# Kernel optimization log

Measured on AMD Instinct MI355X. Metric: run time of the kernel, lower is better.

## Reference

```python
import jax, jax.numpy as jnp
import numpy as np

WS = 7          # window_size
NUM_HEADS = 8
EPS = 1e-5


def _layernorm(x, g, b):
    m = jnp.mean(x, axis=-1, keepdims=True)
    v = jnp.var(x, axis=-1, keepdims=True)
    return (x - m) * jax.lax.rsqrt(v + EPS) * g + b


def _window_attention(win, w_qkv, b_qkv, w_proj, b_proj):
    B_, L, C = win.shape
    h = NUM_HEADS
    d = C // h
    scale = d ** -0.5
    qkv = win @ w_qkv.T + b_qkv                      # (B_, L, 3C)
    qkv = qkv.reshape(B_, L, 3, h, d).transpose(2, 0, 3, 1, 4)  # (3, B_, h, L, d)
    q, k, v = qkv[0], qkv[1], qkv[2]
    attn = jnp.einsum('bhld,bhmd->bhlm', q, k) * scale
    attn = jax.nn.softmax(attn, axis=-1)
    out = jnp.einsum('bhlm,bhmd->bhld', attn, v)     # (B_, h, L, d)
    out = out.transpose(0, 2, 1, 3).reshape(B_, L, C)
    return out @ w_proj.T + b_proj


def _forward(x, H, W, g1, b1, w_qkv, b_qkv, w_proj, b_proj, g2, b2,
             w_fc1, b_fc1, w_fc2, b_fc2):
    N, L, C = x.shape
    shortcut = x
    y = _layernorm(x, g1, b1).reshape(N, H, W, C)
    pad_h = (WS - H % WS) % WS
    pad_w = (WS - W % WS) % WS
    y = jnp.pad(y, ((0, 0), (0, pad_h), (0, pad_w), (0, 0)))
    Hp, Wp = H + pad_h, W + pad_w
    # window partition: (N, Hp/WS, WS, Wp/WS, WS, C) -> (N*nW, WS*WS, C)
    y = y.reshape(N, Hp // WS, WS, Wp // WS, WS, C).transpose(0, 1, 3, 2, 4, 5)
    windows = y.reshape(-1, WS * WS, C)
    attn_windows = _window_attention(windows, w_qkv, b_qkv, w_proj, b_proj)
    # window reverse
    y = attn_windows.reshape(N, Hp // WS, Wp // WS, WS, WS, C)
    y = y.transpose(0, 1, 3, 2, 4, 5).reshape(N, Hp, Wp, C)[:, :H, :W, :]
    y = y.reshape(N, H * W, C)
    x = shortcut + y
    # MLP: Linear -> GELU (erf, torch default) -> Linear
    z = _layernorm(x, g2, b2)
    z = jax.nn.gelu(z @ w_fc1.T + b_fc1, approximate=False) @ w_fc2.T + b_fc2
    return x + z


def setup_inputs() -> dict:
    key = jax.random.key(0)
    ks = jax.random.split(key, 8)
    N, H, W, C = 8, 112, 112, 256
    hidden = 4 * C
    s = 0.02
    return {
        'x': jax.random.normal(ks[0], (N, H * W, C), jnp.float32),
        'H': H,
        'W': W,
        'g1': jnp.ones((C,), jnp.float32),
        'b1': jnp.zeros((C,), jnp.float32),
        'w_qkv': jax.random.normal(ks[1], (3 * C, C), jnp.float32) * s,
        'b_qkv': jnp.zeros((3 * C,), jnp.float32),
        'w_proj': jax.random.normal(ks[2], (C, C), jnp.float32) * s,
        'b_proj': jnp.zeros((C,), jnp.float32),
        'g2': jnp.ones((C,), jnp.float32),
        'b2': jnp.zeros((C,), jnp.float32),
        'w_fc1': jax.random.normal(ks[3], (hidden, C), jnp.float32) * s,
        'b_fc1': jnp.zeros((hidden,), jnp.float32),
        'w_fc2': jax.random.normal(ks[4], (C, hidden), jnp.float32) * s,
        'b_fc2': jnp.zeros((C,), jnp.float32),
    }


def reference(x, H, W, g1, b1, w_qkv, b_qkv, w_proj, b_proj, g2, b2,
              w_fc1, b_fc1, w_fc2, b_fc2):
    return _forward(x, H, W, g1, b1, w_qkv, b_qkv, w_proj, b_proj,
                    g2, b2, w_fc1, b_fc1, w_fc2, b_fc2)
```

## Files before the change

### kernel.cpp

```cpp
#include <hip/hip_runtime.h>
#include <hip/hip_bf16.h>
#include <cstdint>
#include <cstddef>


typedef __bf16 bf16x8 __attribute__((ext_vector_type(8)));
typedef float f32x4 __attribute__((ext_vector_type(4)));

__device__ __forceinline__ unsigned short f2bf(float f){
    union{float f;uint32_t u;}c;c.f=f;uint32_t u=c.u;u+=0x7fffu+((u>>16)&1u);return (unsigned short)(u>>16);}
__device__ __forceinline__ float gelu_f(float x){ return 0.5f*x*(1.0f+erff(x*0.70710678118654752f)); }
__device__ __forceinline__ int swz(int row,int g){ return (g & ~7) | ((g ^ row) & 7); }

__global__ __launch_bounds__(256) void conv_k(
    const float* __restrict__ src, unsigned short* __restrict__ dst, int n4)
{
    int i = blockIdx.x * 256 + threadIdx.x;
    if (i >= n4) return;
    float4 v = *(const float4*)(src + (size_t)i * 4);
    uint2 o;
    o.x = (uint32_t)f2bf(v.x) | ((uint32_t)f2bf(v.y) << 16);
    o.y = (uint32_t)f2bf(v.z) | ((uint32_t)f2bf(v.w) << 16);
    *(uint2*)(dst + (size_t)i * 4) = o;
}

__global__ __launch_bounds__(512, 2) void attn_half_k(
    const float* __restrict__ x, const float* __restrict__ g1, const float* __restrict__ b1,
    const unsigned short* __restrict__ Wqkv, const float* __restrict__ bqkv,
    const unsigned short* __restrict__ Wproj, const float* __restrict__ bproj,
    float* __restrict__ out)
{
    __shared__ __align__(16) unsigned short yb[64 * 256];
    __shared__ __align__(16) unsigned short qkb[64 * 512];
    __shared__ __align__(16) unsigned short vtb[256 * 64];
    const int t = threadIdx.x, lane = t & 63, w = t >> 6;
    const int quad = lane >> 4, l16 = lane & 15;
    const int widx = blockIdx.x;
    const int img = widx >> 8, wi = widx & 255;
    const int wy = wi >> 4, wx = wi & 15;
    const size_t ibase = (size_t)img * 12544;

    for (int tok = w; tok < 49; tok += 8) {
        int r = tok / 7, c = tok - r * 7;
        size_t gtok = ibase + (size_t)(wy * 7 + r) * 112 + (wx * 7 + c);
        float4 v = *(const float4*)(x + gtok * 256 + lane * 4);
        float s = v.x + v.y + v.z + v.w;
        float q = v.x*v.x + v.y*v.y + v.z*v.z + v.w*v.w;
        #pragma unroll
        for (int o = 32; o > 0; o >>= 1) { s += __shfl_xor(s, o); q += __shfl_xor(q, o); }
        float mean = s * (1.f/256.f), var = q * (1.f/256.f) - mean * mean;
        float inv = rsqrtf(var + 1e-5f);
        float4 gv = *(const float4*)(g1 + lane * 4);
        float4 bv = *(const float4*)(b1 + lane * 4);
        uint2 pk;
        pk.x = (uint32_t)f2bf((v.x-mean)*inv*gv.x+bv.x) | ((uint32_t)f2bf((v.y-mean)*inv*gv.y+bv.y) << 16);
        pk.y = (uint32_t)f2bf((v.z-mean)*inv*gv.z+bv.z) | ((uint32_t)f2bf((v.w-mean)*inv*gv.w+bv.w) << 16);
        *(uint2*)&yb[tok*256 + swz(tok, lane >> 1)*8 + (lane & 1)*4] = pk;
    }
    {
        uint2 z2; z2.x = 0u; z2.y = 0u;
        for (int i = t; i < 960; i += 512) {
            int row = 49 + (i >> 6), c4 = (i & 63) * 4;
            *(uint2*)&yb[row*256 + c4] = z2;
        }
    }
    __syncthreads();

    for (int nc = 0; nc < 2; ++nc) {
        const int n0 = nc * 384 + w * 48;
        f32x4 acc[4][3] = {};
        #pragma unroll
        for (int ks = 0; ks < 8; ++ks) {
            bf16x8 af[4], bfr[3];
            #pragma unroll
            for (int mt = 0; mt < 4; ++mt) {
                int m = mt * 16 + l16;
                af[mt] = *(const bf16x8*)&yb[m*256 + swz(m, ks*4 + quad)*8];
            }
            #pragma unroll
            for (int nt = 0; nt < 3; ++nt) {
                int n = n0 + nt * 16 + l16;
                bfr[nt] = *(const bf16x8*)(Wqkv + (size_t)n*256 + ks*32 + quad*8);
            }
            #pragma unroll
            for (int mt = 0; mt < 4; ++mt)
                #pragma unroll
                for (int nt = 0; nt < 3; ++nt)
                    acc[mt][nt] = __builtin_amdgcn_mfma_f32_16x16x32_bf16(
                        af[mt], bfr[nt], acc[mt][nt], 0, 0, 0);
        }
        #pragma unroll
        for (int mt = 0; mt < 4; ++mt)
            #pragma unroll
            for (int nt = 0; nt < 3; ++nt) {
                int col = n0 + nt * 16 + l16;
                float bb = bqkv[col];
                #pragma unroll
                for (int r = 0; r < 4; ++r) {
                    int row = mt * 16 + quad * 4 + r;
                    unsigned short val = f2bf(acc[mt][nt][r] + bb);
                    if (col < 512)
                        qkb[row*512 + swz(row, col >> 3)*8 + (col & 7)] = val;
                    else
                        vtb[(col - 512)*64 + swz(col - 512, row >> 3)*8 + (row & 7)] = val;
                }
            }
    }
    __syncthreads();

    {
        const float scale = 0.17677669529663687f;
        const int h = w;
        unsigned short* pbuf = &yb[w * 2048];

        bf16x8 aq[4], bk[4];
        #pragma unroll
        for (int mt = 0; mt < 4; ++mt) {
            int m = mt * 16 + l16;
            aq[mt] = *(const bf16x8*)&qkb[m*512 + swz(m, h*4 + quad)*8];
        }
        #pragma unroll
        for (int nt = 0; nt < 4; ++nt) {
            int n = nt * 16 + l16;
            bk[nt] = *(const bf16x8*)&qkb[n*512 + swz(n, 32 + h*4 + quad)*8];
        }
        f32x4 s[4][4] = {};
        #pragma unroll
        for (int mt = 0; mt < 4; ++mt)
            #pragma unroll
            for (int nt = 0; nt < 4; ++nt)
                s[mt][nt] = __builtin_amdgcn_mfma_f32_16x16x32_bf16(
                    aq[mt], bk[nt], s[mt][nt], 0, 0, 0);

        uint32_t pk01[4][4], pk23[4][4];
        #pragma unroll
        for (int mt = 0; mt < 4; ++mt)
            #pragma unroll
            for (int r = 0; r < 4; ++r) {
                float v0 = s[mt][0][r];
                float v1 = s[mt][1][r];
                float v2 = s[mt][2][r];
                float v3 = (l16 == 0) ? s[mt][3][r] : -1e30f;
                float mxv = fmaxf(fmaxf(v0, v1), fmaxf(v2, v3));
                #pragma unroll
                for (int off = 8; off > 0; off >>= 1) mxv = fmaxf(mxv, __shfl_xor(mxv, off));
                float p0 = __expf((v0 - mxv) * scale);
                float p1 = __expf((v1 - mxv) * scale);
                float p2 = __expf((v2 - mxv) * scale);
                float p3 = __expf((v3 - mxv) * scale);
                float ssum = p0 + p1 + p2 + p3;
                #pragma unroll
                for (int off = 8; off > 0; off >>= 1) ssum += __shfl_xor(ssum, off);
                float inv = 1.f / ssum;
                pk01[mt][r] = (uint32_t)f2bf(p0*inv) | ((uint32_t)f2bf(p1*inv) << 16);
                pk23[mt][r] = (uint32_t)f2bf(p2*inv) | ((uint32_t)f2bf(p3*inv) << 16);
            }

        f32x4 o[4][2] = {};
        #pragma unroll
        for (int kst = 0; kst < 2; ++kst) {
            #pragma unroll
            for (int mt = 0; mt < 4; ++mt)
                #pragma unroll
                for (int r = 0; r < 4; ++r) {
                    int row = mt * 16 + quad * 4 + r;
                    uint32_t pw = kst ? pk23[mt][r] : pk01[mt][r];
                    int c0 = l16;
                    int c1 = 16 + l16;
                    pbuf[row*32 + (((c0 >> 3) ^ row) & 3)*8 + (c0 & 7)] = (unsigned short)(pw & 0xffffu);
                    pbuf[row*32 + (((c1 >> 3) ^ row) & 3)*8 + (c1 & 7)] = (unsigned short)(pw >> 16);
                }
            bf16x8 ap[4], bv[2];
            #pragma unroll
            for (int mt = 0; mt < 4; ++mt) {
                int m = mt * 16 + l16;
                ap[mt] = *(const bf16x8*)&pbuf[m*32 + ((quad ^ m) & 3)*8];
            }
            #pragma unroll
            for (int nt = 0; nt < 2; ++nt) {
                int c = h*32 + nt*16 + l16;
                bv[nt] = *(const bf16x8*)&vtb[c*64 + swz(c, kst*4 + quad)*8];
            }
            #pragma unroll
            for (int mt = 0; mt < 4; ++mt)
                #pragma unroll
                for (int nt = 0; nt < 2; ++nt)
                    o[mt][nt] = __builtin_amdgcn_mfma_f32_16x16x32_bf16(
                        ap[mt], bv[nt], o[mt][nt], 0, 0, 0);
        }
        #pragma unroll
        for (int mt = 0; mt < 4; ++mt)
            #pragma unroll
            for (int nt = 0; nt < 2; ++nt)
                #pragma unroll
                for (int r = 0; r < 4; ++r) {
                    int row = mt * 16 + quad * 4 + r;
                    int ch = h*32 + nt*16 + l16;
                    float val = (row < 49) ? o[mt][nt][r] : 0.f;
                    qkb[row*512 + swz(row, ch >> 3)*8 + (ch & 7)] = f2bf(val);
                }
    }
    __syncthreads();

    {
        const int n0 = w * 32;
        f32x4 acc[4][2] = {};
        #pragma unroll
        for (int ks = 0; ks < 8; ++ks) {
            bf16x8 af[4], bfr[2];
            #pragma unroll
            for (int mt = 0; mt < 4; ++mt) {
                int m = mt * 16 + l16;
                af[mt] = *(const bf16x8*)&qkb[m*512 + swz(m, ks*4 + quad)*8];
            }
            #pragma unroll
            for (int nt = 0; nt < 2; ++nt) {
                int n = n0 + nt * 16 + l16;
                bfr[nt] = *(const bf16x8*)(Wproj + (size_t)n*256 + ks*32 + quad*8);
            }
            #pragma unroll
            for (int mt = 0; mt < 4; ++mt)
                #pragma unroll
                for (int nt = 0; nt < 2; ++nt)
                    acc[mt][nt] = __builtin_amdgcn_mfma_f32_16x16x32_bf16(
                        af[mt], bfr[nt], acc[mt][nt], 0, 0, 0);
        }
        #pragma unroll
        for (int mt = 0; mt < 4; ++mt)
            #pragma unroll
            for (int r = 0; r < 4; ++r) {
                int row = mt * 16 + quad * 4 + r;
                if (row < 49) {
                    int rr = row / 7, cc = row - rr * 7;
                    size_t gtok = ibase + (size_t)(wy * 7 + rr) * 112 + (wx * 7 + cc);
                    #pragma unroll
                    for (int nt = 0; nt < 2; ++nt) {
                        int col = n0 + nt * 16 + l16;
                        out[gtok * 256 + col] = acc[mt][nt][r] + bproj[col] + x[gtok * 256 + col];
                    }
                }
            }
    }
}

__global__ __launch_bounds__(512, 4) void mlp_half_k(
    const float* __restrict__ g2, const float* __restrict__ b2,
    const unsigned short* __restrict__ W1, const float* __restrict__ bf1,
    const unsigned short* __restrict__ W2, const float* __restrict__ bf2,
    float* __restrict__ out)
{
    __shared__ __align__(16) unsigned short zb[64 * 256];
    __shared__ __align__(16) unsigned short hb[64 * 256];
    const int t = threadIdx.x, lane = t & 63, w = t >> 6;
    const int quad = lane >> 4, l16 = lane & 15;
    const size_t m0 = (size_t)blockIdx.x * 64;

    for (int tok = w; tok < 64; tok += 8) {
        size_t row = m0 + tok;
        float4 v = *(const float4*)&out[row*256 + lane*4];
        float s = v.x+v.y+v.z+v.w, q = v.x*v.x+v.y*v.y+v.z*v.z+v.w*v.w;
        #pragma unroll
        for (int o = 32; o > 0; o >>= 1) { s += __shfl_xor(s, o); q += __shfl_xor(q, o); }
        float mean = s*(1.f/256.f), var = q*(1.f/256.f) - mean*mean;
        float inv = rsqrtf(var + 1e-5f);
        float4 gv = *(const float4*)(g2 + lane*4);
        float4 bv = *(const float4*)(b2 + lane*4);
        uint2 pk;
        pk.x = (uint32_t)f2bf((v.x-mean)*inv*gv.x+bv.x) | ((uint32_t)f2bf((v.y-mean)*inv*gv.y+bv.y) << 16);
        pk.y = (uint32_t)f2bf((v.z-mean)*inv*gv.z+bv.z) | ((uint32_t)f2bf((v.w-mean)*inv*gv.w+bv.w) << 16);
        *(uint2*)&zb[tok*256 + swz(tok, lane >> 1)*8 + (lane & 1)*4] = pk;
    }
    __syncthreads();

    f32x4 acc2[4][2] = {};
    for (int c = 0; c < 4; ++c) {
        const int hc0 = c * 256;
        f32x4 acc1[4][2] = {};
        #pragma unroll
        for (int ks = 0; ks < 8; ++ks) {
            bf16x8 af[4], bfr[2];
            #pragma unroll
            for (int mt = 0; mt < 4; ++mt) {
                int m = mt * 16 + l16;
                af[mt] = *(const bf16x8*)&zb[m*256 + swz(m, ks*4 + quad)*8];
            }
            #pragma unroll
            for (int nt = 0; nt < 2; ++nt) {
                int n = hc0 + w * 32 + nt * 16 + l16;
                bfr[nt] = *(const bf16x8*)(W1 + (size_t)n*256 + ks*32 + quad*8);
            }
            #pragma unroll
            for (int mt = 0; mt < 4; ++mt)
                #pragma unroll
                for (int nt = 0; nt < 2; ++nt)
                    acc1[mt][nt] = __builtin_amdgcn_mfma_f32_16x16x32_bf16(
                        af[mt], bfr[nt], acc1[mt][nt], 0, 0, 0);
        }
        __syncthreads();
        #pragma unroll
        for (int mt = 0; mt < 4; ++mt)
            #pragma unroll
            for (int nt = 0; nt < 2; ++nt) {
                int lc = w * 32 + nt * 16 + l16;
                float bb = bf1[hc0 + lc];
                #pragma unroll
                for (int r = 0; r < 4; ++r) {
                    int row = mt * 16 + quad * 4 + r;
                    hb[row*256 + swz(row, lc >> 3)*8 + (lc & 7)] =
                        f2bf(gelu_f(acc1[mt][nt][r] + bb));
                }
            }
        __syncthreads();
        #pragma unroll
        for (int ks = 0; ks < 8; ++ks) {
            bf16x8 af[4], bfr[2];
            #pragma unroll
            for (int mt = 0; mt < 4; ++mt) {
                int m = mt * 16 + l16;
                af[mt] = *(const bf16x8*)&hb[m*256 + swz(m, ks*4 + quad)*8];
            }
            #pragma unroll
            for (int nt = 0; nt < 2; ++nt) {
                int n = w * 32 + nt * 16 + l16;
                bfr[nt] = *(const bf16x8*)(W2 + (size_t)n*1024 + hc0 + ks*32 + quad*8);
            }
            #pragma unroll
            for (int mt = 0; mt < 4; ++mt)
                #pragma unroll
                for (int nt = 0; nt < 2; ++nt)
                    acc2[mt][nt] = __builtin_amdgcn_mfma_f32_16x16x32_bf16(
                        af[mt], bfr[nt], acc2[mt][nt], 0, 0, 0);
        }
    }
    #pragma unroll
    for (int mt = 0; mt < 4; ++mt)
        #pragma unroll
        for (int nt = 0; nt < 2; ++nt) {
            int col = w * 32 + nt * 16 + l16;
            float bb = bf2[col];
            #pragma unroll
            for (int r = 0; r < 4; ++r) {
                size_t row = m0 + mt * 16 + quad * 4 + r;
                out[row*256 + col] = acc2[mt][nt][r] + bb + out[row*256 + col];
            }
        }
}

extern "C" void kernel_launch(void* const* d_in, const int* in_sizes, int n_in,
                              void* d_out, int out_size, void* d_ws, size_t ws_size,
                              hipStream_t stream)
{
    const float* x      = (const float*)d_in[0];
    const float* g1     = (const float*)d_in[3];
    const float* b1     = (const float*)d_in[4];
    const float* w_qkv  = (const float*)d_in[5];
    const float* b_qkv  = (const float*)d_in[6];
    const float* w_proj = (const float*)d_in[7];
    const float* b_proj = (const float*)d_in[8];
    const float* g2     = (const float*)d_in[9];
    const float* b2     = (const float*)d_in[10];
    const float* w_fc1  = (const float*)d_in[11];
    const float* b_fc1  = (const float*)d_in[12];
    const float* w_fc2  = (const float*)d_in[13];
    const float* b_fc2  = (const float*)d_in[14];
    float* out = (float*)d_out;

    unsigned short* cWqkv  = (unsigned short*)d_ws;
    unsigned short* cWproj = cWqkv  + 196608;
    unsigned short* cWfc1  = cWproj + 65536;
    unsigned short* cWfc2  = cWfc1  + 262144;

    conv_k<<<192, 256, 0, stream>>>(w_qkv,  cWqkv,  49152);
    conv_k<<<64,  256, 0, stream>>>(w_proj, cWproj, 16384);
    conv_k<<<256, 256, 0, stream>>>(w_fc1,  cWfc1,  65536);
    conv_k<<<256, 256, 0, stream>>>(w_fc2,  cWfc2,  65536);

    attn_half_k<<<2048, 512, 0, stream>>>(x, g1, b1, cWqkv, b_qkv, cWproj, b_proj, out);
    mlp_half_k<<<1568, 512, 0, stream>>>(g2, b2, cWfc1, b_fc1, cWfc2, b_fc2, out);
}
```

Before: 759.3 us.

## Double attention block to 1024 threads, splitting work across 16 waves

The window-attention kernel now runs 16 waves per block instead of 8. The QKV GEMM drops its two-pass loop so each wave covers one 48-column slice. Attention splits each head's query rows into two halves across wave pairs, and the projection GEMM gives each wave 16 output columns. The P staging buffer moves into the Q/K shared region with padded rows instead of an XOR swizzle, which needs extra barriers before and after the attention core. This aims to raise per-block parallelism and cut per-wave register pressure. The costs are added synchronization and a launch bound of (1024,4) that may force tighter register limits.

```diff
diff --git a/kernel.cpp b/kernel.cpp
--- a/kernel.cpp
+++ b/kernel.cpp
@@ -24,7 +24,7 @@
     *(uint2*)(dst + (size_t)i * 4) = o;
 }
 
-__global__ __launch_bounds__(512, 2) void attn_half_k(
+__global__ __launch_bounds__(1024, 4) void attn_half_k(
     const float* __restrict__ x, const float* __restrict__ g1, const float* __restrict__ b1,
     const unsigned short* __restrict__ Wqkv, const float* __restrict__ bqkv,
     const unsigned short* __restrict__ Wproj, const float* __restrict__ bproj,
@@ -40,7 +40,7 @@
     const int wy = wi >> 4, wx = wi & 15;
     const size_t ibase = (size_t)img * 12544;
 
-    for (int tok = w; tok < 49; tok += 8) {
+    for (int tok = w; tok < 49; tok += 16) {
         int r = tok / 7, c = tok - r * 7;
         size_t gtok = ibase + (size_t)(wy * 7 + r) * 112 + (wx * 7 + c);
         float4 v = *(const float4*)(x + gtok * 256 + lane * 4);
@@ -59,15 +59,15 @@
     }
     {
         uint2 z2; z2.x = 0u; z2.y = 0u;
-        for (int i = t; i < 960; i += 512) {
+        for (int i = t; i < 960; i += 1024) {
             int row = 49 + (i >> 6), c4 = (i & 63) * 4;
             *(uint2*)&yb[row*256 + c4] = z2;
         }
     }
     __syncthreads();
 
-    for (int nc = 0; nc < 2; ++nc) {
-        const int n0 = nc * 384 + w * 48;
+    {
+        const int n0 = w * 48;
         f32x4 acc[4][3] = {};
         #pragma unroll
         for (int ks = 0; ks < 8; ++ks) {
@@ -110,37 +110,39 @@
 
     {
         const float scale = 0.17677669529663687f;
-        const int h = w;
-        unsigned short* pbuf = &yb[w * 2048];
-
-        bf16x8 aq[4], bk[4];
-        #pragma unroll
-        for (int mt = 0; mt < 4; ++mt) {
-            int m = mt * 16 + l16;
-            aq[mt] = *(const bf16x8*)&qkb[m*512 + swz(m, h*4 + quad)*8];
+        const int h = w & 7, half = w >> 3;
+        unsigned short* pbuf = qkb + w * 1280;
+
+        bf16x8 aq[2], bk[4];
+        #pragma unroll
+        for (int mtl = 0; mtl < 2; ++mtl) {
+            int m = half*32 + mtl*16 + l16;
+            aq[mtl] = *(const bf16x8*)&qkb[m*512 + swz(m, h*4 + quad)*8];
         }
         #pragma unroll
         for (int nt = 0; nt < 4; ++nt) {
             int n = nt * 16 + l16;
             bk[nt] = *(const bf16x8*)&qkb[n*512 + swz(n, 32 + h*4 + quad)*8];
         }
-        f32x4 s[4][4] = {};
-        #pragma unroll
-        for (int mt = 0; mt < 4; ++mt)
+        __syncthreads();
+
+        f32x4 s[2][4] = {};
+        #pragma unroll
+        for (int mtl = 0; mtl < 2; ++mtl)
             #pragma unroll
             for (int nt = 0; nt < 4; ++nt)
-                s[mt][nt] = __builtin_amdgcn_mfma_f32_16x16x32_bf16(
-                    aq[mt], bk[nt], s[mt][nt], 0, 0, 0);
-
-        uint32_t pk01[4][4], pk23[4][4];
-        #pragma unroll
-        for (int mt = 0; mt < 4; ++mt)
+                s[mtl][nt] = __builtin_amdgcn_mfma_f32_16x16x32_bf16(
+                    aq[mtl], bk[nt], s[mtl][nt], 0, 0, 0);
+
+        uint32_t pk01[2][4], pk23[2][4];
+        #pragma unroll
+        for (int mtl = 0; mtl < 2; ++mtl)
             #pragma unroll
             for (int r = 0; r < 4; ++r) {
-                float v0 = s[mt][0][r];
-                float v1 = s[mt][1][r];
-                float v2 = s[mt][2][r];
-                float v3 = (l16 == 0) ? s[mt][3][r] : -1e30f;
+                float v0 = s[mtl][0][r];
+                float v1 = s[mtl][1][r];
+                float v2 = s[mtl][2][r];
+                float v3 = (l16 == 0) ? s[mtl][3][r] : -1e30f;
                 float mxv = fmaxf(fmaxf(v0, v1), fmaxf(v2, v3));
                 #pragma unroll
                 for (int off = 8; off > 0; off >>= 1) mxv = fmaxf(mxv, __shfl_xor(mxv, off));
@@ -152,29 +154,27 @@
                 #pragma unroll
                 for (int off = 8; off > 0; off >>= 1) ssum += __shfl_xor(ssum, off);
                 float inv = 1.f / ssum;
-                pk01[mt][r] = (uint32_t)f2bf(p0*inv) | ((uint32_t)f2bf(p1*inv) << 16);
-                pk23[mt][r] = (uint32_t)f2bf(p2*inv) | ((uint32_t)f2bf(p3*inv) << 16);
-            }
-
-        f32x4 o[4][2] = {};
+                pk01[mtl][r] = (uint32_t)f2bf(p0*inv) | ((uint32_t)f2bf(p1*inv) << 16);
+                pk23[mtl][r] = (uint32_t)f2bf(p2*inv) | ((uint32_t)f2bf(p3*inv) << 16);
+            }
+
+        f32x4 o[2][2] = {};
         #pragma unroll
         for (int kst = 0; kst < 2; ++kst) {
             #pragma unroll
-            for (int mt = 0; mt < 4; ++mt)
+            for (int mtl = 0; mtl < 2; ++mtl)
                 #pragma unroll
                 for (int r = 0; r < 4; ++r) {
-                    int row = mt * 16 + quad * 4 + r;
-                    uint32_t pw = kst ? pk23[mt][r] : pk01[mt][r];
-                    int c0 = l16;
-                    int c1 = 16 + l16;
-                    pbuf[row*32 + (((c0 >> 3) ^ row) & 3)*8 + (c0 & 7)] = (unsigned short)(pw & 0xffffu);
-                    pbuf[row*32 + (((c1 >> 3) ^ row) & 3)*8 + (c1 & 7)] = (unsigned short)(pw >> 16);
-                }
-            bf16x8 ap[4], bv[2];
-            #pragma unroll
-            for (int mt = 0; mt < 4; ++mt) {
-                int m = mt * 16 + l16;
-                ap[mt] = *(const bf16x8*)&pbuf[m*32 + ((quad ^ m) & 3)*8];
+                    int lr = mtl*16 + quad*4 + r;
+                    uint32_t pw = kst ? pk23[mtl][r] : pk01[mtl][r];
+                    pbuf[lr*40 + l16]      = (unsigned short)(pw & 0xffffu);
+                    pbuf[lr*40 + 16 + l16] = (unsigned short)(pw >> 16);
+                }
+            bf16x8 ap[2], bv[2];
+            #pragma unroll
+            for (int mtl = 0; mtl < 2; ++mtl) {
+                int m = mtl * 16 + l16;
+                ap[mtl] = *(const bf16x8*)&pbuf[m*40 + quad*8];
             }
             #pragma unroll
             for (int nt = 0; nt < 2; ++nt) {
@@ -182,48 +182,49 @@
                 bv[nt] = *(const bf16x8*)&vtb[c*64 + swz(c, kst*4 + quad)*8];
             }
             #pragma unroll
-            for (int mt = 0; mt < 4; ++mt)
+            for (int mtl = 0; mtl < 2; ++mtl)
                 #pragma unroll
                 for (int nt = 0; nt < 2; ++nt)
-                    o[mt][nt] = __builtin_amdgcn_mfma_f32_16x16x32_bf16(
-                        ap[mt], bv[nt], o[mt][nt], 0, 0, 0);
-        }
-        #pragma unroll
-        for (int mt = 0; mt < 4; ++mt)
+                    o[mtl][nt] = __builtin_amdgcn_mfma_f32_16x16x32_bf16(
+                        ap[mtl], bv[nt], o[mtl][nt], 0, 0, 0);
+        }
+        __syncthreads();
+
+        #pragma unroll
+        for (int mtl = 0; mtl < 2; ++mtl)
             #pragma unroll
             for (int nt = 0; nt < 2; ++nt)
                 #pragma unroll
                 for (int r = 0; r < 4; ++r) {
-                    int row = mt * 16 + quad * 4 + r;
+                    int row = half*32 + mtl*16 + quad*4 + r;
                     int ch = h*32 + nt*16 + l16;
-                    float val = (row < 49) ? o[mt][nt][r] : 0.f;
+                    float val = (row < 49) ? o[mtl][nt][r] : 0.f;
                     qkb[row*512 + swz(row, ch >> 3)*8 + (ch & 7)] = f2bf(val);
                 }
     }
     __syncthreads();
 
     {
-        const int n0 = w * 32;
-        f32x4 acc[4][2] = {};
+        const int n0 = w * 16;
+        f32x4 acc[4];
+        #pragma unroll
+        for (int mt = 0; mt < 4; ++mt) acc[mt] = (f32x4){0.f,0.f,0.f,0.f};
         #pragma unroll
         for (int ks = 0; ks < 8; ++ks) {
-            bf16x8 af[4], bfr[2];
+            bf16x8 af[4], bfr;
             #pragma unroll
             for (int mt = 0; mt < 4; ++mt) {
                 int m = mt * 16 + l16;
                 af[mt] = *(const bf16x8*)&qkb[m*512 + swz(m, ks*4 + quad)*8];
             }
-            #pragma unroll
-            for (int nt = 0; nt < 2; ++nt) {
-                int n = n0 + nt * 16 + l16;
-                bfr[nt] = *(const bf16x8*)(Wproj + (size_t)n*256 + ks*32 + quad*8);
+            {
+                int n = n0 + l16;
+                bfr = *(const bf16x8*)(Wproj + (size_t)n*256 + ks*32 + quad*8);
             }
             #pragma unroll
             for (int mt = 0; mt < 4; ++mt)
-                #pragma unroll
-                for (int nt = 0; nt < 2; ++nt)
-                    acc[mt][nt] = __builtin_amdgcn_mfma_f32_16x16x32_bf16(
-                        af[mt], bfr[nt], acc[mt][nt], 0, 0, 0);
+                acc[mt] = __builtin_amdgcn_mfma_f32_16x16x32_bf16(
+                    af[mt], bfr, acc[mt], 0, 0, 0);
         }
         #pragma unroll
         for (int mt = 0; mt < 4; ++mt)
@@ -233,11 +234,8 @@
                 if (row < 49) {
                     int rr = row / 7, cc = row - rr * 7;
                     size_t gtok = ibase + (size_t)(wy * 7 + rr) * 112 + (wx * 7 + cc);
-                    #pragma unroll
-                    for (int nt = 0; nt < 2; ++nt) {
-                        int col = n0 + nt * 16 + l16;
-                        out[gtok * 256 + col] = acc[mt][nt][r] + bproj[col] + x[gtok * 256 + col];
-                    }
+                    int col = n0 + l16;
+                    out[gtok * 256 + col] = acc[mt][r] + bproj[col] + x[gtok * 256 + col];
                 }
             }
     }
@@ -375,6 +373,6 @@
     conv_k<<<256, 256, 0, stream>>>(w_fc1,  cWfc1,  65536);
     conv_k<<<256, 256, 0, stream>>>(w_fc2,  cWfc2,  65536);
 
-    attn_half_k<<<2048, 512, 0, stream>>>(x, g1, b1, cWqkv, b_qkv, cWproj, b_proj, out);
+    attn_half_k<<<2048, 1024, 0, stream>>>(x, g1, b1, cWqkv, b_qkv, cWproj, b_proj, out);
     mlp_half_k<<<1568, 512, 0, stream>>>(g2, b2, cWfc1, b_fc1, cWfc2, b_fc2, out);
 }
```

Measured after the change: 716.0 us. 5.7% less time.
